# Kernel optimization log

Hardware: AMD Instinct MI355X
Metric: run time of the kernel (lower is better)

The kernel has to match this reference:

```python
import jax, jax.numpy as jnp
import numpy as np

T, B = 64, 64
E, H, V, L = 512, 1024, 32000, 2


def setup_inputs() -> dict:
    key = jax.random.key(0)
    ks = jax.random.split(key, 16)
    s = 0.05  # weight scale for numerical sanity
    return {
        "dec_input": jax.random.randint(ks[0], (T, B), 0, V),
        "enc_outputs": jax.random.normal(ks[1], (B, 48, H), jnp.float32),
        "h0": jax.random.normal(ks[2], (L, B, H), jnp.float32),
        "c0": jax.random.normal(ks[3], (L, B, H), jnp.float32),
        "emb_W": jax.random.normal(ks[4], (V, E), jnp.float32) * s,
        "W_ih0": jax.random.normal(ks[5], (4 * H, E), jnp.float32) * s,
        "W_hh0": jax.random.normal(ks[6], (4 * H, H), jnp.float32) * s,
        "b_ih0": jax.random.normal(ks[7], (4 * H,), jnp.float32) * s,
        "b_hh0": jax.random.normal(ks[8], (4 * H,), jnp.float32) * s,
        "W_ih1": jax.random.normal(ks[9], (4 * H, H), jnp.float32) * s,
        "W_hh1": jax.random.normal(ks[10], (4 * H, H), jnp.float32) * s,
        "b_ih1": jax.random.normal(ks[11], (4 * H,), jnp.float32) * s,
        "b_hh1": jax.random.normal(ks[12], (4 * H,), jnp.float32) * s,
        "W_out": jax.random.normal(ks[13], (V, H), jnp.float32) * s,
        "b_out": jax.random.normal(ks[14], (V,), jnp.float32) * s,
    }


def _lstm_cell(x, h, c, Wih, Whh, bih, bhh):
    # PyTorch LSTMCell gate order: i, f, g, o
    g = x @ Wih.T + bih + h @ Whh.T + bhh  # [B, 4H]
    i, f, gg, o = jnp.split(g, 4, axis=-1)
    c_n = jax.nn.sigmoid(f) * c + jax.nn.sigmoid(i) * jnp.tanh(gg)
    h_n = jax.nn.sigmoid(o) * jnp.tanh(c_n)
    return h_n, c_n


def reference(dec_input, enc_outputs, h0, c0, emb_W,
              W_ih0, W_hh0, b_ih0, b_hh0,
              W_ih1, W_hh1, b_ih1, b_hh1,
              W_out, b_out):
    emb = emb_W[dec_input]            # [T, B, E]
    xs = emb[:-1]                     # inputs for steps 0..T-2
    tgt = dec_input[1:]               # gather targets dec_input[t+1]

    def step(carry, inp):
        h, c, loss = carry            # h,c: [L, B, H]
        x, t = inp
        h0n, c0n = _lstm_cell(x, h[0], c[0], W_ih0, W_hh0, b_ih0, b_hh0)
        h1n, c1n = _lstm_cell(h0n, h[1], c[1], W_ih1, W_hh1, b_ih1, b_hh1)
        logits = h1n @ W_out.T + b_out              # [B, V]
        lp = jax.nn.log_softmax(logits, axis=-1)
        loss = loss - jnp.take_along_axis(lp, t[:, None], axis=1).sum()
        return (jnp.stack([h0n, h1n]), jnp.stack([c0n, c1n]), loss), None

    init = (h0, c0, jnp.zeros((), h0.dtype))
    (_, _, loss), _ = jax.lax.scan(step, init, (xs, tgt))
    return loss
```

## Files before the change

kernel.cpp:

```cpp
#include <hip/hip_runtime.h>
#include <hip/hip_cooperative_groups.h>
#include <math.h>

#define TSTEPS 63
#define BB 64
#define ED 512
#define HD 1024
#define VV 32000
#define GG 4096
#define NROWS 4032
#define MPAD 4096
#define NCH 500
#define HSLOT 65536

typedef __attribute__((ext_vector_type(8))) short short8;
typedef __attribute__((ext_vector_type(4))) float f32x4;

__device__ __forceinline__ float sigf(float x) { return 1.0f / (1.0f + __expf(-x)); }

__device__ __forceinline__ short f2bf(float f) {
  unsigned u = __float_as_uint(f);
  unsigned r = (u + 0x7FFFu + ((u >> 16) & 1u)) >> 16;
  return (short)r;
}
__device__ __forceinline__ float bf2f(short h) {
  return __uint_as_float(((unsigned)(unsigned short)h) << 16);
}

#define GLOAD_LDS(g, l) \
  __builtin_amdgcn_global_load_lds((const __attribute__((address_space(1))) void*)(g), \
                                   (__attribute__((address_space(3))) void*)(l), 16, 0, 0)

__global__ __launch_bounds__(256)
void cvt_f2b_k(const float* __restrict__ src, short* __restrict__ dst) {
  int i = (blockIdx.x * 256 + threadIdx.x) * 4;
  float4 v = *(const float4*)(src + i);
  short4 o;
  o.x = f2bf(v.x); o.y = f2bf(v.y); o.z = f2bf(v.z); o.w = f2bf(v.w);
  *(short4*)(dst + i) = o;
}

__global__ __launch_bounds__(256)
void gather_emb_k(const int* __restrict__ dec, const float* __restrict__ emb,
                  short* __restrict__ XembB) {
  int idx = blockIdx.x * 256 + threadIdx.x;
  int r = idx >> 7, cc = (idx & 127) * 4;
  int src = dec[r];
  float4 v = *(const float4*)(emb + (size_t)src * ED + cc);
  short4 o;
  o.x = f2bf(v.x); o.y = f2bf(v.y); o.z = f2bf(v.z); o.w = f2bf(v.w);
  *(short4*)(XembB + (size_t)r * ED + cc) = o;
}

__global__ __launch_bounds__(256)
void init_state2_k(const float* __restrict__ h0, const float* __restrict__ c0,
                   short* __restrict__ h0buf, short* __restrict__ H1b,
                   float* __restrict__ c0s, float* __restrict__ c1s) {
  int i = blockIdx.x * 256 + threadIdx.x;
  h0buf[HSLOT + i] = f2bf(h0[i]);
  H1b[i] = f2bf(h0[BB * HD + i]);
  c0s[i] = c0[i];
  c1s[i] = c0[BB * HD + i];
}

__global__ __launch_bounds__(256)
void bias_sum_k(const float* __restrict__ a, const float* __restrict__ b,
                float* __restrict__ s) {
  int i = blockIdx.x * 256 + threadIdx.x;
  s[i] = a[i] + b[i];
}

__global__ __launch_bounds__(256)
void pad_h1b_k(short* __restrict__ dst) {
  int i = (blockIdx.x * 256 + threadIdx.x) * 4;
  short4 z; z.x = z.y = z.z = z.w = 0;
  *(short4*)(dst + i) = z;
}

__global__ void zero_out_k(float* __restrict__ out) {
  if (threadIdx.x == 0) out[0] = 0.f;
}

template<int NK>
__device__ __forceinline__ void mfma_loop(const short* __restrict__ Abase, int lda,
                                          const short* __restrict__ Bbase, int ldb,
                                          short* lds_a, short* lds_b,
                                          f32x4 acc[4][4]) {
  const int tid = threadIdx.x;
  const int l = tid & 63;
  const int w = tid >> 6;
  const int wm = w >> 1, wn = w & 1;
  const int p = tid & 7;
  const int rbase = tid >> 3;

  for (int kt = 0; kt < NK; kt++) {
#pragma unroll
    for (int it = 0; it < 4; it++) {
      int row = it * 32 + rbase;
      int ch = p ^ (row & 7);
      const short* ga = Abase + (size_t)row * lda + kt * 64 + ch * 8;
      const short* gb = Bbase + (size_t)row * ldb + kt * 64 + ch * 8;
      short* la = lds_a + it * 2048 + tid * 8;
      short* lb = lds_b + it * 2048 + tid * 8;
      GLOAD_LDS(ga, la);
      GLOAD_LDS(gb, lb);
    }
    asm volatile("s_waitcnt vmcnt(0)" ::: "memory");
    __syncthreads();

    short8 af[4][2], bf[4][2];
#pragma unroll
    for (int m = 0; m < 4; m++) {
#pragma unroll
      for (int ks = 0; ks < 2; ks++) {
        int ra = wm * 64 + m * 16 + (l & 15);
        int ca = (ks * 4 + (l >> 4)) ^ (ra & 7);
        af[m][ks] = *(const short8*)(lds_a + ra * 64 + ca * 8);
        int rb = wn * 64 + m * 16 + (l & 15);
        int cb = (ks * 4 + (l >> 4)) ^ (rb & 7);
        bf[m][ks] = *(const short8*)(lds_b + rb * 64 + cb * 8);
      }
    }
#pragma unroll
    for (int ks = 0; ks < 2; ks++)
#pragma unroll
      for (int m = 0; m < 4; m++)
#pragma unroll
        for (int n = 0; n < 4; n++)
          acc[m][n] = __builtin_amdgcn_mfma_f32_16x16x32_bf16(af[m][ks], bf[n][ks],
                                                              acc[m][n], 0, 0, 0);
    __syncthreads();
  }
}

__global__ __launch_bounds__(256)
void x0_mfma_k(const short* __restrict__ XembB, const short* __restrict__ Wih0B,
               const float* __restrict__ bih0, const float* __restrict__ bhh0,
               float* __restrict__ X0) {
  __shared__ short lds_a[128 * 64];
  __shared__ short lds_b[128 * 64];
  f32x4 acc[4][4];
#pragma unroll
  for (int m = 0; m < 4; m++)
#pragma unroll
    for (int n = 0; n < 4; n++)
#pragma unroll
      for (int q = 0; q < 4; q++) acc[m][n][q] = 0.f;

  mfma_loop<8>(XembB + (size_t)blockIdx.x * 128 * ED, ED,
               Wih0B + (size_t)blockIdx.y * 128 * ED, ED, lds_a, lds_b, acc);

  const int l = threadIdx.x & 63;
  const int w = threadIdx.x >> 6;
  const int wm = w >> 1, wn = w & 1;
#pragma unroll
  for (int m = 0; m < 4; m++)
#pragma unroll
    for (int r = 0; r < 4; r++) {
      int row = blockIdx.x * 128 + wm * 64 + m * 16 + (l >> 4) * 4 + r;
#pragma unroll
      for (int n = 0; n < 4; n++) {
        int col = blockIdx.y * 128 + wn * 64 + n * 16 + (l & 15);
        X0[(size_t)row * GG + col] = acc[m][n][r] + bih0[col] + bhh0[col];
      }
    }
}

__global__ __launch_bounds__(256, 1)
void recurrence_k(const float* __restrict__ X0, const float* __restrict__ bsum1,
                  const short* __restrict__ Wh0b, const short* __restrict__ Wi1b,
                  const short* __restrict__ Wh1b, short* __restrict__ h0buf,
                  short* __restrict__ H1b, float* __restrict__ c0s,
                  float* __restrict__ c1s) {
  cooperative_groups::grid_group grid = cooperative_groups::this_grid();
  __shared__ short lA[2][4096];
  __shared__ short lB[2][8192];
  const int tid = threadIdx.x;
  const int l   = tid & 63;
  const int w   = tid >> 6;
  const int p8  = tid & 7;
  const int r32 = tid >> 3;
  const int lj  = l & 15;
  const int lh  = l >> 4;
  const bool isA = (blockIdx.x < 32);
  const int g = isA ? (int)blockIdx.x : (int)blockIdx.x - 32;

  for (int ph = 0; ph < 64; ph++) {
    if (isA && ph < TSTEPS) {
      const int t = ph;
      const int jb = g * 32;
      const short* Ab = h0buf + ((t + 1) & 1) * HSLOT;
      f32x4 acc[8];
#pragma unroll
      for (int f = 0; f < 8; f++)
#pragma unroll
        for (int q = 0; q < 4; q++) acc[f][q] = 0.f;

      auto stage0 = [&](int kt, int buf) {
#pragma unroll
        for (int it = 0; it < 2; it++) {
          int row = it * 32 + r32;
          int ch = p8 ^ (row & 7);
          GLOAD_LDS(Ab + (size_t)row * HD + kt * 64 + ch * 8,
                    &lA[buf][it * 2048 + tid * 8]);
        }
#pragma unroll
        for (int it = 0; it < 4; it++) {
          int row = it * 32 + r32;
          int grow = (row >> 5) * HD + jb + (row & 31);
          int ch = p8 ^ (row & 7);
          GLOAD_LDS(Wh0b + (size_t)grow * HD + kt * 64 + ch * 8,
                    &lB[buf][it * 2048 + tid * 8]);
        }
      };

      stage0(0, 0);
      __syncthreads();
      for (int kt = 0; kt < 16; kt++) {
        int cur = kt & 1;
        if (kt < 15) stage0(kt + 1, cur ^ 1);
        int ra = w * 16 + lj;
        short8 af[2];
#pragma unroll
        for (int ks = 0; ks < 2; ks++) {
          int ca = (ks * 4 + lh) ^ (ra & 7);
          af[ks] = *(const short8*)&lA[cur][ra * 64 + ca * 8];
        }
#pragma unroll
        for (int f = 0; f < 8; f++) {
          int rb = f * 16 + lj;
#pragma unroll
          for (int ks = 0; ks < 2; ks++) {
            int cb = (ks * 4 + lh) ^ (rb & 7);
            short8 bfr = *(const short8*)&lB[cur][rb * 64 + cb * 8];
            acc[f] = __builtin_amdgcn_mfma_f32_16x16x32_bf16(af[ks], bfr, acc[f], 0, 0, 0);
          }
        }
        __syncthreads();
      }
      const float* X0t = X0 + (size_t)t * BB * GG;
      short* hdst = h0buf + (t & 1) * HSLOT;
#pragma unroll
      for (int jj = 0; jj < 2; jj++) {
        int j = jb + jj * 16 + lj;
#pragma unroll
        for (int r = 0; r < 4; r++) {
          int b = w * 16 + lh * 4 + r;
          float gi = acc[0 + jj][r] + X0t[(size_t)b * GG + j];
          float gf = acc[2 + jj][r] + X0t[(size_t)b * GG + HD + j];
          float gg = acc[4 + jj][r] + X0t[(size_t)b * GG + 2 * HD + j];
          float go = acc[6 + jj][r] + X0t[(size_t)b * GG + 3 * HD + j];
          float cp = c0s[b * HD + j];
          float cn = sigf(gf) * cp + sigf(gi) * tanhf(gg);
          float hn = sigf(go) * tanhf(cn);
          c0s[b * HD + j] = cn;
          hdst[b * HD + j] = f2bf(hn);
        }
      }
    } else if (!isA && ph >= 1) {
      const int t = ph - 1;
      const int jb = g * 16;
      f32x4 acc[4];
#pragma unroll
      for (int f = 0; f < 4; f++)
#pragma unroll
        for (int q = 0; q < 4; q++) acc[f][q] = 0.f;

      auto stage1 = [&](int u, int buf) {
        int seg = u >> 4, kt = u & 15;
        const short* Ab = seg ? (H1b + (size_t)t * HSLOT) : (h0buf + (t & 1) * HSLOT);
        const short* Wb = seg ? Wh1b : Wi1b;
#pragma unroll
        for (int it = 0; it < 2; it++) {
          int row = it * 32 + r32;
          int ch = p8 ^ (row & 7);
          GLOAD_LDS(Ab + (size_t)row * HD + kt * 64 + ch * 8,
                    &lA[buf][it * 2048 + tid * 8]);
          int grow = (row >> 4) * HD + jb + (row & 15);
          GLOAD_LDS(Wb + (size_t)grow * HD + kt * 64 + ch * 8,
                    &lB[buf][it * 2048 + tid * 8]);
        }
      };

      stage1(0, 0);
      __syncthreads();
      for (int u = 0; u < 32; u++) {
        int cur = u & 1;
        if (u < 31) stage1(u + 1, cur ^ 1);
        int ra = w * 16 + lj;
        short8 af[2];
#pragma unroll
        for (int ks = 0; ks < 2; ks++) {
          int ca = (ks * 4 + lh) ^ (ra & 7);
          af[ks] = *(const short8*)&lA[cur][ra * 64 + ca * 8];
        }
#pragma unroll
        for (int f = 0; f < 4; f++) {
          int rb = f * 16 + lj;
#pragma unroll
          for (int ks = 0; ks < 2; ks++) {
            int cb = (ks * 4 + lh) ^ (rb & 7);
            short8 bfr = *(const short8*)&lB[cur][rb * 64 + cb * 8];
            acc[f] = __builtin_amdgcn_mfma_f32_16x16x32_bf16(af[ks], bfr, acc[f], 0, 0, 0);
          }
        }
        __syncthreads();
      }
      int j = jb + lj;
      short* hdst = H1b + (size_t)(t + 1) * HSLOT;
#pragma unroll
      for (int r = 0; r < 4; r++) {
        int b = w * 16 + lh * 4 + r;
        float gi = acc[0][r] + bsum1[j];
        float gf = acc[1][r] + bsum1[HD + j];
        float gg = acc[2][r] + bsum1[2 * HD + j];
        float go = acc[3][r] + bsum1[3 * HD + j];
        float cp = c1s[b * HD + j];
        float cn = sigf(gf) * cp + sigf(gi) * tanhf(gg);
        float hn = sigf(go) * tanhf(cn);
        c1s[b * HD + j] = cn;
        hdst[b * HD + j] = f2bf(hn);
      }
    }
    __threadfence();
    grid.sync();
  }
}

__global__ __launch_bounds__(256)
void tgt_logit_k(const short* __restrict__ H1log, const float* __restrict__ Wout,
                 const float* __restrict__ bout, const int* __restrict__ dec,
                 float* __restrict__ tl) {
  int gw = (blockIdx.x * 256 + threadIdx.x) >> 6;
  int lane = threadIdx.x & 63;
  if (gw >= NROWS) return;
  int tgt = dec[gw + 64];
  const short* hrow = H1log + (size_t)gw * HD;
  const float* wrow = Wout + (size_t)tgt * HD;
  float s = 0.f;
#pragma unroll
  for (int q = 0; q < 16; q++) {
    int k = lane + q * 64;
    s += bf2f(hrow[k]) * wrow[k];
  }
#pragma unroll
  for (int off = 32; off > 0; off >>= 1) s += __shfl_down(s, off);
  if (lane == 0) tl[gw] = s + bout[tgt];
}

__global__ __launch_bounds__(256)
void lse_mfma_k(const short* __restrict__ H1log, const short* __restrict__ WoutB,
                const float* __restrict__ bout, float* __restrict__ m_part,
                float* __restrict__ s_part) {
  __shared__ short lds_a[128 * 64];
  __shared__ short lds_b[128 * 64];
  f32x4 acc[4][4];
#pragma unroll
  for (int m = 0; m < 4; m++)
#pragma unroll
    for (int n = 0; n < 4; n++)
#pragma unroll
      for (int q = 0; q < 4; q++) acc[m][n][q] = 0.f;

  mfma_loop<16>(H1log + (size_t)blockIdx.x * 128 * HD, HD,
                WoutB + (size_t)blockIdx.y * 128 * HD, HD, lds_a, lds_b, acc);

  const int l = threadIdx.x & 63;
  const int w = threadIdx.x >> 6;
  const int wm = w >> 1, wn = w & 1;
  const int colbase = blockIdx.y * 128 + wn * 64 + (l & 15);
  float bo[4];
#pragma unroll
  for (int n = 0; n < 4; n++) bo[n] = bout[colbase + n * 16];
  const int ch = blockIdx.y * 2 + wn;

#pragma unroll
  for (int m = 0; m < 4; m++) {
#pragma unroll
    for (int r = 0; r < 4; r++) {
      float v0 = acc[m][0][r] + bo[0];
      float v1 = acc[m][1][r] + bo[1];
      float v2 = acc[m][2][r] + bo[2];
      float v3 = acc[m][3][r] + bo[3];
      float mx = fmaxf(fmaxf(v0, v1), fmaxf(v2, v3));
      float s = __expf(v0 - mx) + __expf(v1 - mx) + __expf(v2 - mx) + __expf(v3 - mx);
#pragma unroll
      for (int off = 1; off < 16; off <<= 1) {
        float mo = __shfl_xor(mx, off);
        float so = __shfl_xor(s, off);
        float nm = fmaxf(mx, mo);
        s = s * __expf(mx - nm) + so * __expf(mo - nm);
        mx = nm;
      }
      if ((l & 15) == 0) {
        int row = blockIdx.x * 128 + wm * 64 + m * 16 + (l >> 4) * 4 + r;
        m_part[(size_t)ch * MPAD + row] = mx;
        s_part[(size_t)ch * MPAD + row] = s;
      }
    }
  }
}

__global__ __launch_bounds__(256)
void row_lse_k(const float* __restrict__ m_part, const float* __restrict__ s_part,
               const float* __restrict__ tl, float* __restrict__ out) {
  int row = blockIdx.x * 256 + threadIdx.x;
  float loss = 0.f;
  if (row < NROWS) {
    float M = -INFINITY, S = 0.f;
    for (int ch = 0; ch < NCH; ch++) {
      float m = m_part[(size_t)ch * MPAD + row];
      float s = s_part[(size_t)ch * MPAD + row];
      float nm = fmaxf(M, m);
      S = S * __expf(M - nm) + s * __expf(m - nm);
      M = nm;
    }
    loss = M + logf(S) - tl[row];
  }
  __shared__ float red[256];
  red[threadIdx.x] = loss;
  __syncthreads();
  for (int s = 128; s > 0; s >>= 1) {
    if (threadIdx.x < s) red[threadIdx.x] += red[threadIdx.x + s];
    __syncthreads();
  }
  if (threadIdx.x == 0) atomicAdd(out, red[0]);
}

extern "C" void kernel_launch(void* const* d_in, const int* in_sizes, int n_in,
                              void* d_out, int out_size, void* d_ws, size_t ws_size,
                              hipStream_t stream) {
  const int*   dec  = (const int*)  d_in[0];
  const float* h0   = (const float*)d_in[2];
  const float* c0   = (const float*)d_in[3];
  const float* emb  = (const float*)d_in[4];
  const float* Wih0 = (const float*)d_in[5];
  const float* Whh0 = (const float*)d_in[6];
  const float* bih0 = (const float*)d_in[7];
  const float* bhh0 = (const float*)d_in[8];
  const float* Wih1 = (const float*)d_in[9];
  const float* Whh1 = (const float*)d_in[10];
  const float* bih1 = (const float*)d_in[11];
  const float* bhh1 = (const float*)d_in[12];
  const float* Wout = (const float*)d_in[13];
  const float* bout = (const float*)d_in[14];
  float* out = (float*)d_out;

  float* ws = (float*)d_ws;
  float* X0     = ws;
  float* m_part = X0 + (size_t)MPAD * GG;
  float* s_part = m_part + (size_t)NCH * MPAD;
  float* tl     = s_part + (size_t)NCH * MPAD;
  float* c0s    = tl + MPAD;
  float* c1s    = c0s + BB * HD;
  float* bsum1  = c1s + BB * HD;
  short* H1b    = (short*)(bsum1 + GG);
  short* WoutB  = H1b + HSLOT + (size_t)MPAD * HD;
  short* Wih0B  = WoutB + (size_t)VV * HD;
  short* XembB  = Wih0B + (size_t)GG * ED;
  short* Wh0b   = XembB + (size_t)MPAD * ED;
  short* Wi1b   = Wh0b + (size_t)GG * HD;
  short* Wh1b   = Wi1b + (size_t)GG * HD;
  short* h0buf  = Wh1b + (size_t)GG * HD;
  short* H1log  = H1b + HSLOT;

  cvt_f2b_k<<<(VV * HD) / 1024, 256, 0, stream>>>(Wout, WoutB);
  cvt_f2b_k<<<(GG * ED) / 1024, 256, 0, stream>>>(Wih0, Wih0B);
  cvt_f2b_k<<<(GG * HD) / 1024, 256, 0, stream>>>(Whh0, Wh0b);
  cvt_f2b_k<<<(GG * HD) / 1024, 256, 0, stream>>>(Wih1, Wi1b);
  cvt_f2b_k<<<(GG * HD) / 1024, 256, 0, stream>>>(Whh1, Wh1b);
  gather_emb_k<<<(MPAD * ED / 4) / 256, 256, 0, stream>>>(dec, emb, XembB);
  init_state2_k<<<256, 256, 0, stream>>>(h0, c0, h0buf, H1b, c0s, c1s);
  bias_sum_k<<<16, 256, 0, stream>>>(bih1, bhh1, bsum1);
  pad_h1b_k<<<64, 256, 0, stream>>>(H1log + (size_t)NROWS * HD);
  zero_out_k<<<1, 64, 0, stream>>>(out);
  x0_mfma_k<<<dim3(MPAD / 128, GG / 128), 256, 0, stream>>>(XembB, Wih0B, bih0, bhh0, X0);

  void* args[] = {&X0, &bsum1, &Wh0b, &Wi1b, &Wh1b, &h0buf, &H1b, &c0s, &c1s};
  hipLaunchCooperativeKernel((void*)recurrence_k, dim3(96), dim3(256), args, 0, stream);

  tgt_logit_k<<<(NROWS * 64 + 255) / 256, 256, 0, stream>>>(H1log, Wout, bout, dec, tl);
  lse_mfma_k<<<dim3(MPAD / 128, VV / 128), 256, 0, stream>>>(H1log, WoutB, bout, m_part, s_part);
  row_lse_k<<<MPAD / 256, 256, 0, stream>>>(m_part, s_part, tl, out);
}
```

Baseline: 3.543 ms.

## Restructure LSTM recurrence: 128 blocks, direct-register MFMA loads, cell state in registers

The cooperative recurrence kernel now runs 64 blocks per layer instead of 32+64, each owning 16 hidden units. Each wave handles one gate and loads A and B fragments straight from global memory into registers with software double-buffering, dropping the LDS staging and per-k-tile barriers. Gate results are exchanged through a small shared buffer, and cell state is kept in registers across all timesteps instead of being read and written in global memory. This spreads the work over more CUs and cuts synchronisation per step, at the cost of uncoalesced direct global loads and redundant reads of the activation matrix across waves.

```diff
diff --git a/kernel.cpp b/kernel.cpp
--- a/kernel.cpp
+++ b/kernel.cpp
@@ -53,14 +53,11 @@
 }
 
 __global__ __launch_bounds__(256)
-void init_state2_k(const float* __restrict__ h0, const float* __restrict__ c0,
-                   short* __restrict__ h0buf, short* __restrict__ H1b,
-                   float* __restrict__ c0s, float* __restrict__ c1s) {
+void init_state2_k(const float* __restrict__ h0, short* __restrict__ h0buf,
+                   short* __restrict__ H1b) {
   int i = blockIdx.x * 256 + threadIdx.x;
   h0buf[HSLOT + i] = f2bf(h0[i]);
   H1b[i] = f2bf(h0[BB * HD + i]);
-  c0s[i] = c0[i];
-  c1s[i] = c0[BB * HD + i];
 }
 
 __global__ __launch_bounds__(256)
@@ -170,155 +167,145 @@
 void recurrence_k(const float* __restrict__ X0, const float* __restrict__ bsum1,
                   const short* __restrict__ Wh0b, const short* __restrict__ Wi1b,
                   const short* __restrict__ Wh1b, short* __restrict__ h0buf,
-                  short* __restrict__ H1b, float* __restrict__ c0s,
-                  float* __restrict__ c1s) {
+                  short* __restrict__ H1b, const float* __restrict__ c0all) {
   cooperative_groups::grid_group grid = cooperative_groups::this_grid();
-  __shared__ short lA[2][4096];
-  __shared__ short lB[2][8192];
+  __shared__ float Gs[64][4][16];
   const int tid = threadIdx.x;
-  const int l   = tid & 63;
-  const int w   = tid >> 6;
-  const int p8  = tid & 7;
-  const int r32 = tid >> 3;
-  const int lj  = l & 15;
-  const int lh  = l >> 4;
-  const bool isA = (blockIdx.x < 32);
-  const int g = isA ? (int)blockIdx.x : (int)blockIdx.x - 32;
+  const int l  = tid & 63;
+  const int w  = tid >> 6;
+  const int li = l & 15;
+  const int kc = l >> 4;
+  const bool isL0 = (blockIdx.x < 64);
+  const int g  = isL0 ? (int)blockIdx.x : (int)blockIdx.x - 64;
+  const int jb = g * 16;
+
+  const int cc = tid & 15, bq = tid >> 4;
+  float creg[4];
+#pragma unroll
+  for (int r = 0; r < 4; r++)
+    creg[r] = c0all[(isL0 ? 0 : BB * HD) + (size_t)(r * 16 + bq) * HD + jb + cc];
+
+  const short* Wb0 = Wh0b + (size_t)(w * HD + jb) * HD;
+  const short* Wi1w = Wi1b + (size_t)(w * HD + jb) * HD;
+  const short* Wh1w = Wh1b + (size_t)(w * HD + jb) * HD;
 
   for (int ph = 0; ph < 64; ph++) {
-    if (isA && ph < TSTEPS) {
+    if (isL0 && ph < TSTEPS) {
       const int t = ph;
-      const int jb = g * 32;
-      const short* Ab = h0buf + ((t + 1) & 1) * HSLOT;
-      f32x4 acc[8];
-#pragma unroll
-      for (int f = 0; f < 8; f++)
-#pragma unroll
-        for (int q = 0; q < 4; q++) acc[f][q] = 0.f;
-
-      auto stage0 = [&](int kt, int buf) {
-#pragma unroll
-        for (int it = 0; it < 2; it++) {
-          int row = it * 32 + r32;
-          int ch = p8 ^ (row & 7);
-          GLOAD_LDS(Ab + (size_t)row * HD + kt * 64 + ch * 8,
-                    &lA[buf][it * 2048 + tid * 8]);
+      const short* Ap = h0buf + ((t + 1) & 1) * HSLOT;
+      f32x4 acc[4];
+#pragma unroll
+      for (int m = 0; m < 4; m++)
+#pragma unroll
+        for (int q = 0; q < 4; q++) acc[m][q] = 0.f;
+
+      short8 aE[4], aO[4], bE, bO;
+#pragma unroll
+      for (int m = 0; m < 4; m++)
+        aE[m] = *(const short8*)(Ap + (size_t)(m * 16 + li) * HD + kc * 8);
+      bE = *(const short8*)(Wb0 + (size_t)li * HD + kc * 8);
+#pragma unroll
+      for (int kt = 0; kt < 32; kt += 2) {
+#pragma unroll
+        for (int m = 0; m < 4; m++)
+          aO[m] = *(const short8*)(Ap + (size_t)(m * 16 + li) * HD + (kt + 1) * 32 + kc * 8);
+        bO = *(const short8*)(Wb0 + (size_t)li * HD + (kt + 1) * 32 + kc * 8);
+#pragma unroll
+        for (int m = 0; m < 4; m++)
+          acc[m] = __builtin_amdgcn_mfma_f32_16x16x32_bf16(aE[m], bE, acc[m], 0, 0, 0);
+        if (kt + 2 < 32) {
+#pragma unroll
+          for (int m = 0; m < 4; m++)
+            aE[m] = *(const short8*)(Ap + (size_t)(m * 16 + li) * HD + (kt + 2) * 32 + kc * 8);
+          bE = *(const short8*)(Wb0 + (size_t)li * HD + (kt + 2) * 32 + kc * 8);
         }
 #pragma unroll
-        for (int it = 0; it < 4; it++) {
-          int row = it * 32 + r32;
-          int grow = (row >> 5) * HD + jb + (row & 31);
-          int ch = p8 ^ (row & 7);
-          GLOAD_LDS(Wh0b + (size_t)grow * HD + kt * 64 + ch * 8,
-                    &lB[buf][it * 2048 + tid * 8]);
-        }
-      };
-
-      stage0(0, 0);
+        for (int m = 0; m < 4; m++)
+          acc[m] = __builtin_amdgcn_mfma_f32_16x16x32_bf16(aO[m], bO, acc[m], 0, 0, 0);
+      }
+#pragma unroll
+      for (int m = 0; m < 4; m++)
+#pragma unroll
+        for (int r = 0; r < 4; r++)
+          Gs[m * 16 + kc * 4 + r][w][li] = acc[m][r];
       __syncthreads();
-      for (int kt = 0; kt < 16; kt++) {
-        int cur = kt & 1;
-        if (kt < 15) stage0(kt + 1, cur ^ 1);
-        int ra = w * 16 + lj;
-        short8 af[2];
-#pragma unroll
-        for (int ks = 0; ks < 2; ks++) {
-          int ca = (ks * 4 + lh) ^ (ra & 7);
-          af[ks] = *(const short8*)&lA[cur][ra * 64 + ca * 8];
-        }
-#pragma unroll
-        for (int f = 0; f < 8; f++) {
-          int rb = f * 16 + lj;
-#pragma unroll
-          for (int ks = 0; ks < 2; ks++) {
-            int cb = (ks * 4 + lh) ^ (rb & 7);
-            short8 bfr = *(const short8*)&lB[cur][rb * 64 + cb * 8];
-            acc[f] = __builtin_amdgcn_mfma_f32_16x16x32_bf16(af[ks], bfr, acc[f], 0, 0, 0);
-          }
-        }
-        __syncthreads();
-      }
+
       const float* X0t = X0 + (size_t)t * BB * GG;
       short* hdst = h0buf + (t & 1) * HSLOT;
-#pragma unroll
-      for (int jj = 0; jj < 2; jj++) {
-        int j = jb + jj * 16 + lj;
-#pragma unroll
-        for (int r = 0; r < 4; r++) {
-          int b = w * 16 + lh * 4 + r;
-          float gi = acc[0 + jj][r] + X0t[(size_t)b * GG + j];
-          float gf = acc[2 + jj][r] + X0t[(size_t)b * GG + HD + j];
-          float gg = acc[4 + jj][r] + X0t[(size_t)b * GG + 2 * HD + j];
-          float go = acc[6 + jj][r] + X0t[(size_t)b * GG + 3 * HD + j];
-          float cp = c0s[b * HD + j];
-          float cn = sigf(gf) * cp + sigf(gi) * tanhf(gg);
-          float hn = sigf(go) * tanhf(cn);
-          c0s[b * HD + j] = cn;
-          hdst[b * HD + j] = f2bf(hn);
+      const int j = jb + cc;
+#pragma unroll
+      for (int r = 0; r < 4; r++) {
+        int b = r * 16 + bq;
+        float gi = Gs[b][0][cc] + X0t[(size_t)b * GG + j];
+        float gf = Gs[b][1][cc] + X0t[(size_t)b * GG + HD + j];
+        float gg = Gs[b][2][cc] + X0t[(size_t)b * GG + 2 * HD + j];
+        float go = Gs[b][3][cc] + X0t[(size_t)b * GG + 3 * HD + j];
+        float cn = sigf(gf) * creg[r] + sigf(gi) * tanhf(gg);
+        float hn = sigf(go) * tanhf(cn);
+        creg[r] = cn;
+        hdst[b * HD + j] = f2bf(hn);
+      }
+    } else if (!isL0 && ph >= 1) {
+      const int t = ph - 1;
+      const short* A0b = h0buf + (t & 1) * HSLOT;
+      const short* A1b = H1b + (size_t)t * HSLOT;
+      f32x4 acc[4];
+#pragma unroll
+      for (int m = 0; m < 4; m++)
+#pragma unroll
+        for (int q = 0; q < 4; q++) acc[m][q] = 0.f;
+
+      short8 aE[4], aO[4], bE, bO;
+#pragma unroll
+      for (int m = 0; m < 4; m++)
+        aE[m] = *(const short8*)(A0b + (size_t)(m * 16 + li) * HD + kc * 8);
+      bE = *(const short8*)(Wi1w + (size_t)li * HD + kc * 8);
+#pragma unroll
+      for (int kt = 0; kt < 64; kt += 2) {
+        {
+          const short* ab = (kt + 1 < 32) ? A0b : A1b;
+          const short* wb = (kt + 1 < 32) ? Wi1w : Wh1w;
+          int kk = (kt + 1) & 31;
+#pragma unroll
+          for (int m = 0; m < 4; m++)
+            aO[m] = *(const short8*)(ab + (size_t)(m * 16 + li) * HD + kk * 32 + kc * 8);
+          bO = *(const short8*)(wb + (size_t)li * HD + kk * 32 + kc * 8);
         }
-      }
-    } else if (!isA && ph >= 1) {
-      const int t = ph - 1;
-      const int jb = g * 16;
-      f32x4 acc[4];
-#pragma unroll
-      for (int f = 0; f < 4; f++)
-#pragma unroll
-        for (int q = 0; q < 4; q++) acc[f][q] = 0.f;
-
-      auto stage1 = [&](int u, int buf) {
-        int seg = u >> 4, kt = u & 15;
-        const short* Ab = seg ? (H1b + (size_t)t * HSLOT) : (h0buf + (t & 1) * HSLOT);
-        const short* Wb = seg ? Wh1b : Wi1b;
-#pragma unroll
-        for (int it = 0; it < 2; it++) {
-          int row = it * 32 + r32;
-          int ch = p8 ^ (row & 7);
-          GLOAD_LDS(Ab + (size_t)row * HD + kt * 64 + ch * 8,
-                    &lA[buf][it * 2048 + tid * 8]);
-          int grow = (row >> 4) * HD + jb + (row & 15);
-          GLOAD_LDS(Wb + (size_t)grow * HD + kt * 64 + ch * 8,
-                    &lB[buf][it * 2048 + tid * 8]);
+#pragma unroll
+        for (int m = 0; m < 4; m++)
+          acc[m] = __builtin_amdgcn_mfma_f32_16x16x32_bf16(aE[m], bE, acc[m], 0, 0, 0);
+        if (kt + 2 < 64) {
+          const short* ab = (kt + 2 < 32) ? A0b : A1b;
+          const short* wb = (kt + 2 < 32) ? Wi1w : Wh1w;
+          int kk = (kt + 2) & 31;
+#pragma unroll
+          for (int m = 0; m < 4; m++)
+            aE[m] = *(const short8*)(ab + (size_t)(m * 16 + li) * HD + kk * 32 + kc * 8);
+          bE = *(const short8*)(wb + (size_t)li * HD + kk * 32 + kc * 8);
         }
-      };
-
-      stage1(0, 0);
+#pragma unroll
+        for (int m = 0; m < 4; m++)
+          acc[m] = __builtin_amdgcn_mfma_f32_16x16x32_bf16(aO[m], bO, acc[m], 0, 0, 0);
+      }
+#pragma unroll
+      for (int m = 0; m < 4; m++)
+#pragma unroll
+        for (int r = 0; r < 4; r++)
+          Gs[m * 16 + kc * 4 + r][w][li] = acc[m][r];
       __syncthreads();
-      for (int u = 0; u < 32; u++) {
-        int cur = u & 1;
-        if (u < 31) stage1(u + 1, cur ^ 1);
-        int ra = w * 16 + lj;
-        short8 af[2];
-#pragma unroll
-        for (int ks = 0; ks < 2; ks++) {
-          int ca = (ks * 4 + lh) ^ (ra & 7);
-          af[ks] = *(const short8*)&lA[cur][ra * 64 + ca * 8];
-        }
-#pragma unroll
-        for (int f = 0; f < 4; f++) {
-          int rb = f * 16 + lj;
-#pragma unroll
-          for (int ks = 0; ks < 2; ks++) {
-            int cb = (ks * 4 + lh) ^ (rb & 7);
-            short8 bfr = *(const short8*)&lB[cur][rb * 64 + cb * 8];
-            acc[f] = __builtin_amdgcn_mfma_f32_16x16x32_bf16(af[ks], bfr, acc[f], 0, 0, 0);
-          }
-        }
-        __syncthreads();
-      }
-      int j = jb + lj;
+
       short* hdst = H1b + (size_t)(t + 1) * HSLOT;
+      const int j = jb + cc;
 #pragma unroll
       for (int r = 0; r < 4; r++) {
-        int b = w * 16 + lh * 4 + r;
-        float gi = acc[0][r] + bsum1[j];
-        float gf = acc[1][r] + bsum1[HD + j];
-        float gg = acc[2][r] + bsum1[2 * HD + j];
-        float go = acc[3][r] + bsum1[3 * HD + j];
-        float cp = c1s[b * HD + j];
-        float cn = sigf(gf) * cp + sigf(gi) * tanhf(gg);
+        int b = r * 16 + bq;
+        float gi = Gs[b][0][cc] + bsum1[j];
+        float gf = Gs[b][1][cc] + bsum1[HD + j];
+        float gg = Gs[b][2][cc] + bsum1[2 * HD + j];
+        float go = Gs[b][3][cc] + bsum1[3 * HD + j];
+        float cn = sigf(gf) * creg[r] + sigf(gi) * tanhf(gg);
         float hn = sigf(go) * tanhf(cn);
-        c1s[b * HD + j] = cn;
+        creg[r] = cn;
         hdst[b * HD + j] = f2bf(hn);
       }
     }
@@ -451,9 +438,7 @@
   float* m_part = X0 + (size_t)MPAD * GG;
   float* s_part = m_part + (size_t)NCH * MPAD;
   float* tl     = s_part + (size_t)NCH * MPAD;
-  float* c0s    = tl + MPAD;
-  float* c1s    = c0s + BB * HD;
-  float* bsum1  = c1s + BB * HD;
+  float* bsum1  = tl + MPAD;
   short* H1b    = (short*)(bsum1 + GG);
   short* WoutB  = H1b + HSLOT + (size_t)MPAD * HD;
   short* Wih0B  = WoutB + (size_t)VV * HD;
@@ -470,14 +455,14 @@
   cvt_f2b_k<<<(GG * HD) / 1024, 256, 0, stream>>>(Wih1, Wi1b);
   cvt_f2b_k<<<(GG * HD) / 1024, 256, 0, stream>>>(Whh1, Wh1b);
   gather_emb_k<<<(MPAD * ED / 4) / 256, 256, 0, stream>>>(dec, emb, XembB);
-  init_state2_k<<<256, 256, 0, stream>>>(h0, c0, h0buf, H1b, c0s, c1s);
+  init_state2_k<<<256, 256, 0, stream>>>(h0, h0buf, H1b);
   bias_sum_k<<<16, 256, 0, stream>>>(bih1, bhh1, bsum1);
   pad_h1b_k<<<64, 256, 0, stream>>>(H1log + (size_t)NROWS * HD);
   zero_out_k<<<1, 64, 0, stream>>>(out);
   x0_mfma_k<<<dim3(MPAD / 128, GG / 128), 256, 0, stream>>>(XembB, Wih0B, bih0, bhh0, X0);
 
-  void* args[] = {&X0, &bsum1, &Wh0b, &Wi1b, &Wh1b, &h0buf, &H1b, &c0s, &c1s};
-  hipLaunchCooperativeKernel((void*)recurrence_k, dim3(96), dim3(256), args, 0, stream);
+  void* args[] = {&X0, &bsum1, &Wh0b, &Wi1b, &Wh1b, &h0buf, &H1b, (void*)&c0};
+  hipLaunchCooperativeKernel((void*)recurrence_k, dim3(128), dim3(256), args, 0, stream);
 
   tgt_logit_k<<<(NROWS * 64 + 255) / 256, 256, 0, stream>>>(H1log, Wout, bout, dec, tl);
   lse_mfma_k<<<dim3(MPAD / 128, VV / 128), 256, 0, stream>>>(H1log, WoutB, bout, m_part, s_part);
```

New measurement: 4.705 ms. 32.8% more time.
